# Kernel tuning notes

Measured on AMD Instinct MI355X. Metric: run time of the kernel, lower is better.

## Reference

```python
import jax, jax.numpy as jnp
import numpy as np

V0, V1, C = 64, 128, 128
V = V0 * V1  # product-graph node count = kron eigenvalue count


def setup_inputs() -> dict:
    key = jax.random.key(0)
    ks = jax.random.split(key, 8)
    x = jax.random.normal(ks[0], (V, C), dtype=jnp.float32)
    edge_index = jax.random.randint(ks[1], (2, 100), 0, V)  # unused on spectral path
    L = jnp.zeros((2, 2), dtype=jnp.float32)                # unused on spectral path
    mass = jax.random.uniform(ks[2], (V,), dtype=jnp.float32) + 0.5  # positive lumped mass
    evals0 = jax.random.uniform(ks[3], (V0,), dtype=jnp.float32) * 2.0  # factor-graph eigenvalues >= 0
    evals1 = jax.random.uniform(ks[4], (V1,), dtype=jnp.float32) * 2.0
    evecs = jax.random.normal(ks[5], (V, V), dtype=jnp.float32) / np.float32(np.sqrt(V))
    diffusion_time = jax.random.uniform(ks[6], (2, C), dtype=jnp.float32)  # nn.Parameter [P, C_inout]
    return {
        "x": x, "edge_index": edge_index, "L": L, "mass": mass,
        "evals0": evals0, "evals1": evals1, "evecs": evecs,
        "diffusion_time": diffusion_time,
    }


def reference(x, edge_index, L, mass, evals0, evals1, evecs, diffusion_time):
    # to_basis: project mass-weighted signal onto the spectral basis. [V,C]
    x_spec = evecs.T @ (x * mass[:, None])
    # Per-channel Kronecker diffusion coefficients:
    # kron(exp(-t0[c]*evals0), exp(-t1[c]*evals1)) for each channel c.
    e0 = jnp.exp(-evals0[:, None] * diffusion_time[0][None, :])  # [V0, C]
    e1 = jnp.exp(-evals1[:, None] * diffusion_time[1][None, :])  # [V1, C]
    diffusion_coefs = (e0[:, None, :] * e1[None, :, :]).reshape(V0 * V1, C)  # [V, C]
    # from_basis: back to node domain.
    x_diffuse = evecs @ (diffusion_coefs * x_spec)
    return x_diffuse
```

## Files before the change

### kernel.cpp

```cpp
#include <hip/hip_runtime.h>
#include <stdint.h>

#define V 8192
#define C 128
#define KS 8
#define KCH (V / KS)
#define BK 64
#define NI (KCH / BK)

typedef __attribute__((ext_vector_type(8))) short short8;
typedef __attribute__((ext_vector_type(4))) float floatx4;

static __device__ __forceinline__ unsigned short f2bf(float f) {
    unsigned u = __float_as_uint(f);
    u += 0x7FFF + ((u >> 16) & 1);
    return (unsigned short)(u >> 16);
}

static __device__ __forceinline__ void gload16(const void* g, void* l) {
    __builtin_amdgcn_global_load_lds(
        (const __attribute__((address_space(1))) void*)g,
        (__attribute__((address_space(3))) void*)l, 16, 0, 0);
}
#define SWAIT(s) asm volatile("s_waitcnt " s ::: "memory")
#define SBAR() __builtin_amdgcn_s_barrier()
#define SFENCE() __builtin_amdgcn_sched_barrier(0)

__global__ __launch_bounds__(256) void prep_xmt(const float* __restrict__ x,
                                                const float* __restrict__ mass,
                                                unsigned short* __restrict__ XMT) {
    __shared__ float tile[64][65];
    const int k0 = blockIdx.x * 64;
    const int c0 = blockIdx.y * 64;
    const int t = threadIdx.x;
#pragma unroll
    for (int p = 0; p < 16; ++p) {
        int idx = p * 256 + t;
        int kk = idx >> 6, cc = idx & 63;
        tile[kk][cc] = x[(size_t)(k0 + kk) * C + (c0 + cc)] * mass[k0 + kk];
    }
    __syncthreads();
#pragma unroll
    for (int p = 0; p < 16; ++p) {
        int idx = p * 256 + t;
        int cc = idx >> 6, kk = idx & 63;
        XMT[(size_t)(c0 + cc) * V + (k0 + kk)] = f2bf(tile[kk][cc]);
    }
}

#define MFMA_BODY(pA, pB)                                                           \
    {                                                                               \
        _Pragma("unroll")                                                           \
        for (int kk = 0; kk < BK; kk += 32) {                                       \
            short8 af[4], bfv[4];                                                   \
            _Pragma("unroll")                                                       \
            for (int mi = 0; mi < 4; ++mi) {                                        \
                const int m = wm + mi * 16 + l15;                                   \
                const int cpos = ((kk >> 3) + q) ^ (m & 7);                         \
                af[mi] = *(const short8*)&pA[m * BK + 8 * cpos];                    \
            }                                                                       \
            _Pragma("unroll")                                                       \
            for (int ni = 0; ni < 4; ++ni) {                                        \
                const int n = wn + ni * 16 + l15;                                   \
                const int cpos = ((kk >> 3) + q) ^ (n & 7);                         \
                bfv[ni] = *(const short8*)&pB[n * BK + 8 * cpos];                   \
            }                                                                       \
            _Pragma("unroll")                                                       \
            for (int mi = 0; mi < 4; ++mi)                                          \
                _Pragma("unroll")                                                   \
                for (int ni = 0; ni < 4; ++ni)                                      \
                    acc[mi][ni] = __builtin_amdgcn_mfma_f32_16x16x32_bf16(          \
                        af[mi], bfv[ni], acc[mi][ni], 0, 0, 0);                     \
        }                                                                           \
    }

__global__ __launch_bounds__(256, 2) void gemm1_fused(const unsigned short* __restrict__ XMT,
                                                      const float* __restrict__ E,
                                                      unsigned short* __restrict__ EB,
                                                      float* __restrict__ P1) {
    __shared__ __align__(16) unsigned short ldsA[2][128 * BK];
    __shared__ __align__(16) unsigned short ldsB[2][128 * BK];
    const int bx = blockIdx.x;
    const int ks = bx & (KS - 1);
    const int n0 = (bx >> 3) * 128;
    const int kb = ks * KCH;
    const int t = threadIdx.x;
    const int w = t >> 6, lane = t & 63, q = lane >> 4, l15 = lane & 15;
    const int wm = (w & 1) * 64, wn = (w >> 1) * 64;
    const int lr = lane >> 3;
    const int lch = (lane & 7) ^ lr;
    const int jg = (lane & 7) | (w << 3);
    const int vq = lane >> 3;

    floatx4 acc[4][4] = {};
    float4 er0[8], er1[8];

#define G1_CONV(ER, TI, BUF)                                                        \
    {                                                                               \
        const float* lf = (const float*)ER;                                         \
        unsigned short cv[8][4];                                                    \
        _Pragma("unroll")                                                           \
        for (int rr = 0; rr < 8; ++rr)                                              \
            _Pragma("unroll")                                                       \
            for (int jj = 0; jj < 4; ++jj) cv[rr][jj] = f2bf(lf[rr * 4 + jj]);      \
        _Pragma("unroll")                                                           \
        for (int jj = 0; jj < 4; ++jj) {                                            \
            const int j = jg * 4 + jj;                                              \
            short8 b;                                                               \
            _Pragma("unroll")                                                       \
            for (int rr = 0; rr < 8; ++rr) b[rr] = (short)cv[rr][jj];               \
            *(short8*)&ldsB[BUF][j * BK + (vq ^ (j & 7)) * 8] = b;                  \
        }                                                                           \
        _Pragma("unroll")                                                           \
        for (int rr = 0; rr < 8; ++rr) {                                            \
            ushort4 av;                                                             \
            av.x = cv[rr][0]; av.y = cv[rr][1]; av.z = cv[rr][2]; av.w = cv[rr][3]; \
            *(ushort4*)&EB[(size_t)(kb + (TI) * BK + vq * 8 + rr) * V + n0 + jg * 4] = av; \
        }                                                                           \
    }

#define G1_ELOAD(ER, TI)                                                            \
    {                                                                               \
        const int kk_ = kb + (TI) * BK;                                             \
        _Pragma("unroll")                                                           \
        for (int rr = 0; rr < 8; ++rr)                                              \
            ER[rr] = *(const float4*)&E[(size_t)(kk_ + vq * 8 + rr) * V + n0 + jg * 4]; \
    }

#define G1_GLOADA(TI, BUF)                                                          \
    {                                                                               \
        const int kk_ = kb + (TI) * BK;                                             \
        _Pragma("unroll")                                                           \
        for (int i = 0; i < 4; ++i)                                                 \
            gload16(&XMT[(size_t)(i * 32 + w * 8 + lr) * V + kk_ + 8 * lch],        \
                    &ldsA[BUF][i * 2048 + w * 512]);                                \
    }

    G1_ELOAD(er0, 0);
    G1_GLOADA(0, 0);
    G1_ELOAD(er1, 1);
    G1_CONV(er0, 0, 0);
    SWAIT("vmcnt(16) lgkmcnt(0)");
    SBAR();
    SFENCE();

#define G1_BODY(T, PF_ER, CV_ER)                                                    \
    {                                                                               \
        const int t1 = (T) + 1;                                                     \
        const int t2 = ((T) + 2 < NI) ? (T) + 2 : NI - 1;                           \
        const bool pf = t1 < NI;                                                    \
        if (pf) {                                                                   \
            G1_GLOADA(t1, cur ^ 1);                                                 \
            G1_ELOAD(PF_ER, t2);                                                    \
        }                                                                           \
        SFENCE();                                                                   \
        {                                                                           \
            const unsigned short* pA = ldsA[cur];                                   \
            const unsigned short* pB = ldsB[cur];                                   \
            __builtin_amdgcn_s_setprio(1);                                          \
            MFMA_BODY(pA, pB);                                                      \
            __builtin_amdgcn_s_setprio(0);                                          \
        }                                                                           \
        SFENCE();                                                                   \
        if (pf) {                                                                   \
            G1_CONV(CV_ER, t1, cur ^ 1);                                            \
            SWAIT("vmcnt(16) lgkmcnt(0)");                                          \
            SBAR();                                                                 \
            SFENCE();                                                               \
            cur ^= 1;                                                               \
        }                                                                           \
    }

    int cur = 0;
    for (int tt = 0; tt < NI; tt += 2) {
        G1_BODY(tt, er0, er1);
        G1_BODY(tt + 1, er1, er0);
    }

    float* Pks = P1 + (size_t)ks * C * V;
#pragma unroll
    for (int mi = 0; mi < 4; ++mi) {
        int mrow = wm + mi * 16 + q * 4;
#pragma unroll
        for (int ni = 0; ni < 4; ++ni) {
            int n = n0 + wn + ni * 16 + l15;
#pragma unroll
            for (int r = 0; r < 4; ++r)
                Pks[(size_t)(mrow + r) * V + n] = acc[mi][ni][r];
        }
    }
#undef G1_BODY
#undef G1_CONV
#undef G1_ELOAD
#undef G1_GLOADA
}

__global__ __launch_bounds__(256, 2) void gemm2_fused(const unsigned short* __restrict__ EB,
                                                      const unsigned short* __restrict__ YT,
                                                      float* __restrict__ P2) {
    __shared__ __align__(16) unsigned short ldsA[2][128 * BK];
    __shared__ __align__(16) unsigned short ldsB[2][128 * BK];
    const int bx = blockIdx.x;
    const int ks = bx & (KS - 1);
    const int m0 = (bx >> 3) * 128;
    const int kb = ks * KCH;
    const int t = threadIdx.x;
    const int w = t >> 6, lane = t & 63, q = lane >> 4, l15 = lane & 15;
    const int wm = (w & 1) * 64, wn = (w >> 1) * 64;
    const int lr = lane >> 3;
    const int lch = (lane & 7) ^ lr;

    floatx4 acc[4][4] = {};

#define G2_STAGE(TI, BUF)                                                           \
    {                                                                               \
        const int kk_ = kb + (TI) * BK;                                             \
        _Pragma("unroll")                                                           \
        for (int i = 0; i < 4; ++i)                                                 \
            gload16(&EB[(size_t)(m0 + i * 32 + w * 8 + lr) * V + kk_ + 8 * lch],    \
                    &ldsA[BUF][i * 2048 + w * 512]);                                \
        _Pragma("unroll")                                                           \
        for (int i = 0; i < 4; ++i)                                                 \
            gload16(&YT[(size_t)(i * 32 + w * 8 + lr) * V + kk_ + 8 * lch],         \
                    &ldsB[BUF][i * 2048 + w * 512]);                                \
    }

    G2_STAGE(0, 0);
    SWAIT("vmcnt(0)");
    SBAR();
    SFENCE();

    int cur = 0;
    for (int tt = 0; tt < NI; ++tt) {
        const bool pf = (tt + 1 < NI);
        if (pf) G2_STAGE(tt + 1, cur ^ 1);
        SFENCE();
        {
            const unsigned short* pA = ldsA[cur];
            const unsigned short* pB = ldsB[cur];
            __builtin_amdgcn_s_setprio(1);
            MFMA_BODY(pA, pB);
            __builtin_amdgcn_s_setprio(0);
        }
        SFENCE();
        if (pf) {
            SWAIT("vmcnt(0) lgkmcnt(0)");
            SBAR();
            SFENCE();
            cur ^= 1;
        }
    }
#undef G2_STAGE

    float* Pks = P2 + (size_t)ks * V * C;
#pragma unroll
    for (int mi = 0; mi < 4; ++mi) {
        int mrow = m0 + wm + mi * 16 + q * 4;
#pragma unroll
        for (int ni = 0; ni < 4; ++ni) {
            int n = wn + ni * 16 + l15;
#pragma unroll
            for (int r = 0; r < 4; ++r)
                Pks[(size_t)(mrow + r) * C + n] = acc[mi][ni][r];
        }
    }
}

__global__ __launch_bounds__(256) void red1(const float* __restrict__ P1,
                                            const float* __restrict__ ev0,
                                            const float* __restrict__ ev1,
                                            const float* __restrict__ dt,
                                            unsigned short* __restrict__ YT) {
    int id = blockIdx.x * 256 + threadIdx.x;
    int c = id >> 10;
    int j0 = (id & 1023) * 8;
    float s[8] = {};
#pragma unroll
    for (int ks = 0; ks < KS; ++ks) {
        const float* row = &P1[((size_t)ks * C + c) * V + j0];
        float4 a = *(const float4*)row;
        float4 b = *(const float4*)(row + 4);
        s[0] += a.x; s[1] += a.y; s[2] += a.z; s[3] += a.w;
        s[4] += b.x; s[5] += b.y; s[6] += b.z; s[7] += b.w;
    }
    float t0 = dt[c], t1 = dt[C + c];
    float a0 = ev0[j0 >> 7] * t0;
    short8 yv;
#pragma unroll
    for (int jj = 0; jj < 8; ++jj) {
        float coef = __expf(-(a0 + ev1[(j0 + jj) & 127] * t1));
        yv[jj] = (short)f2bf(s[jj] * coef);
    }
    *(short8*)&YT[(size_t)c * V + j0] = yv;
}

__global__ __launch_bounds__(256) void red2(const float* __restrict__ P2,
                                            float* __restrict__ out) {
    int id = blockIdx.x * 256 + threadIdx.x;
    size_t off = (size_t)id * 4;
    float4 s = {0.f, 0.f, 0.f, 0.f};
#pragma unroll
    for (int ks = 0; ks < KS; ++ks) {
        float4 v = *(const float4*)&P2[(size_t)ks * V * C + off];
        s.x += v.x; s.y += v.y; s.z += v.z; s.w += v.w;
    }
    *(float4*)&out[off] = s;
}

extern "C" void kernel_launch(void* const* d_in, const int* in_sizes, int n_in,
                              void* d_out, int out_size, void* d_ws, size_t ws_size,
                              hipStream_t stream) {
    const float* x    = (const float*)d_in[0];
    const float* mass = (const float*)d_in[3];
    const float* ev0  = (const float*)d_in[4];
    const float* ev1  = (const float*)d_in[5];
    const float* E    = (const float*)d_in[6];
    const float* dt   = (const float*)d_in[7];
    float* out = (float*)d_out;

    unsigned short* XMT = (unsigned short*)d_ws;
    unsigned short* YT  = XMT + (size_t)V * C;
    unsigned short* EB  = YT + (size_t)V * C;
    float* P = (float*)(EB + (size_t)V * V);

    prep_xmt<<<dim3(V / 64, C / 64), 256, 0, stream>>>(x, mass, XMT);
    gemm1_fused<<<(V / 128) * KS, 256, 0, stream>>>(XMT, E, EB, P);
    red1<<<(C * V / 8) / 256, 256, 0, stream>>>(P, ev0, ev1, dt, YT);
    gemm2_fused<<<(V / 128) * KS, 256, 0, stream>>>(EB, YT, P);
    red2<<<(V * C / 4) / 256, 256, 0, stream>>>(P, out);
}
```

Baseline: 451.0 us.

## Replace split-K GEMMs and reductions with full-K narrow-tile GEMMs reading fp32 E

Drops the split-K scheme, the fp32 partial buffers, both reduction kernels and the bf16 copy of evecs. Each GEMM now runs the full K loop over 32-wide output tiles with 512 threads, so 256 blocks cover each GEMM. The diffusion coefficients are applied in the first GEMM's epilogue, and the second GEMM writes the output directly. The trade is that the second GEMM re-reads the fp32 evecs (transposed access) instead of a bf16 copy, and every block runs a longer serial K loop with smaller MFMA tiles per wave.

```diff
diff --git a/kernel.cpp b/kernel.cpp
--- a/kernel.cpp
+++ b/kernel.cpp
@@ -3,10 +3,8 @@
 
 #define V 8192
 #define C 128
-#define KS 8
-#define KCH (V / KS)
 #define BK 64
-#define NI (KCH / BK)
+#define NT (V / BK)
 
 typedef __attribute__((ext_vector_type(8))) short short8;
 typedef __attribute__((ext_vector_type(4))) float floatx4;
@@ -48,123 +46,210 @@
     }
 }
 
-#define MFMA_BODY(pA, pB)                                                           \
-    {                                                                               \
-        _Pragma("unroll")                                                           \
-        for (int kk = 0; kk < BK; kk += 32) {                                       \
-            short8 af[4], bfv[4];                                                   \
-            _Pragma("unroll")                                                       \
-            for (int mi = 0; mi < 4; ++mi) {                                        \
-                const int m = wm + mi * 16 + l15;                                   \
-                const int cpos = ((kk >> 3) + q) ^ (m & 7);                         \
-                af[mi] = *(const short8*)&pA[m * BK + 8 * cpos];                    \
-            }                                                                       \
-            _Pragma("unroll")                                                       \
-            for (int ni = 0; ni < 4; ++ni) {                                        \
-                const int n = wn + ni * 16 + l15;                                   \
-                const int cpos = ((kk >> 3) + q) ^ (n & 7);                         \
-                bfv[ni] = *(const short8*)&pB[n * BK + 8 * cpos];                   \
-            }                                                                       \
-            _Pragma("unroll")                                                       \
-            for (int mi = 0; mi < 4; ++mi)                                          \
-                _Pragma("unroll")                                                   \
-                for (int ni = 0; ni < 4; ++ni)                                      \
-                    acc[mi][ni] = __builtin_amdgcn_mfma_f32_16x16x32_bf16(          \
-                        af[mi], bfv[ni], acc[mi][ni], 0, 0, 0);                     \
-        }                                                                           \
-    }
-
-__global__ __launch_bounds__(256, 2) void gemm1_fused(const unsigned short* __restrict__ XMT,
-                                                      const float* __restrict__ E,
-                                                      unsigned short* __restrict__ EB,
-                                                      float* __restrict__ P1) {
+__global__ __launch_bounds__(512, 2) void gemm1y(const unsigned short* __restrict__ XMT,
+                                                 const float* __restrict__ E,
+                                                 const float* __restrict__ ev0,
+                                                 const float* __restrict__ ev1,
+                                                 const float* __restrict__ dt,
+                                                 unsigned short* __restrict__ YT) {
     __shared__ __align__(16) unsigned short ldsA[2][128 * BK];
-    __shared__ __align__(16) unsigned short ldsB[2][128 * BK];
-    const int bx = blockIdx.x;
-    const int ks = bx & (KS - 1);
-    const int n0 = (bx >> 3) * 128;
-    const int kb = ks * KCH;
+    __shared__ __align__(16) unsigned short ldsB[2][32 * BK];
+    const int j0 = blockIdx.x * 32;
     const int t = threadIdx.x;
     const int w = t >> 6, lane = t & 63, q = lane >> 4, l15 = lane & 15;
-    const int wm = (w & 1) * 64, wn = (w >> 1) * 64;
-    const int lr = lane >> 3;
-    const int lch = (lane & 7) ^ lr;
-    const int jg = (lane & 7) | (w << 3);
-    const int vq = lane >> 3;
-
-    floatx4 acc[4][4] = {};
-    float4 er0[8], er1[8];
-
-#define G1_CONV(ER, TI, BUF)                                                        \
-    {                                                                               \
-        const float* lf = (const float*)ER;                                         \
-        unsigned short cv[8][4];                                                    \
-        _Pragma("unroll")                                                           \
-        for (int rr = 0; rr < 8; ++rr)                                              \
-            _Pragma("unroll")                                                       \
-            for (int jj = 0; jj < 4; ++jj) cv[rr][jj] = f2bf(lf[rr * 4 + jj]);      \
+    const int wr = w >> 1, wc = w & 1;
+    const int lr = lane >> 3, lch = (lane & 7) ^ lr;
+    const int vq4 = t >> 3;
+    const int jgc = t & 7;
+
+    floatx4 acc[2] = {};
+    float4 er0[4], er1[4];
+
+#define G1_GLOADA(TI, BUF)                                                          \
+    {                                                                               \
+        const int kk_ = (TI) * BK;                                                  \
+        _Pragma("unroll")                                                           \
+        for (int i = 0; i < 2; ++i)                                                 \
+            gload16(&XMT[(size_t)(i * 64 + w * 8 + lr) * V + kk_ + 8 * lch],        \
+                    &ldsA[BUF][i * 4096 + w * 512]);                                \
+    }
+#define G1_ELOAD(ER, TI)                                                            \
+    if (w < 2) {                                                                    \
+        const int kk_ = (TI) * BK;                                                  \
+        _Pragma("unroll")                                                           \
+        for (int u = 0; u < 4; ++u)                                                 \
+            ER[u] = *(const float4*)&E[(size_t)(kk_ + vq4 * 4 + u) * V + j0 + jgc * 4]; \
+    }
+#define G1_CONV(ER, BUF)                                                            \
+    if (w < 2) {                                                                    \
         _Pragma("unroll")                                                           \
         for (int jj = 0; jj < 4; ++jj) {                                            \
-            const int j = jg * 4 + jj;                                              \
-            short8 b;                                                               \
-            _Pragma("unroll")                                                       \
-            for (int rr = 0; rr < 8; ++rr) b[rr] = (short)cv[rr][jj];               \
-            *(short8*)&ldsB[BUF][j * BK + (vq ^ (j & 7)) * 8] = b;                  \
-        }                                                                           \
-        _Pragma("unroll")                                                           \
-        for (int rr = 0; rr < 8; ++rr) {                                            \
-            ushort4 av;                                                             \
-            av.x = cv[rr][0]; av.y = cv[rr][1]; av.z = cv[rr][2]; av.w = cv[rr][3]; \
-            *(ushort4*)&EB[(size_t)(kb + (TI) * BK + vq * 8 + rr) * V + n0 + jg * 4] = av; \
-        }                                                                           \
-    }
-
-#define G1_ELOAD(ER, TI)                                                            \
-    {                                                                               \
-        const int kk_ = kb + (TI) * BK;                                             \
-        _Pragma("unroll")                                                           \
-        for (int rr = 0; rr < 8; ++rr)                                              \
-            ER[rr] = *(const float4*)&E[(size_t)(kk_ + vq * 8 + rr) * V + n0 + jg * 4]; \
-    }
-
-#define G1_GLOADA(TI, BUF)                                                          \
-    {                                                                               \
-        const int kk_ = kb + (TI) * BK;                                             \
-        _Pragma("unroll")                                                           \
-        for (int i = 0; i < 4; ++i)                                                 \
-            gload16(&XMT[(size_t)(i * 32 + w * 8 + lr) * V + kk_ + 8 * lch],        \
-                    &ldsA[BUF][i * 2048 + w * 512]);                                \
+            const int j = jgc * 4 + jj;                                             \
+            ushort4 b;                                                              \
+            b.x = f2bf(ER[0][jj]); b.y = f2bf(ER[1][jj]);                           \
+            b.z = f2bf(ER[2][jj]); b.w = f2bf(ER[3][jj]);                           \
+            *(ushort4*)&ldsB[BUF][j * BK + ((vq4 >> 1) ^ (j & 7)) * 8 + (vq4 & 1) * 4] = b; \
+        }                                                                           \
+    }
+#define G1_MFMA(pA, pB)                                                             \
+    {                                                                               \
+        _Pragma("unroll")                                                           \
+        for (int kk = 0; kk < BK; kk += 32) {                                       \
+            short8 af[2], bf1;                                                      \
+            _Pragma("unroll")                                                       \
+            for (int mi = 0; mi < 2; ++mi) {                                        \
+                const int m = wr * 32 + mi * 16 + l15;                              \
+                af[mi] = *(const short8*)&pA[m * BK + 8 * (((kk >> 3) + q) ^ (m & 7))]; \
+            }                                                                       \
+            {                                                                       \
+                const int n = wc * 16 + l15;                                        \
+                bf1 = *(const short8*)&pB[n * BK + 8 * (((kk >> 3) + q) ^ (n & 7))]; \
+            }                                                                       \
+            _Pragma("unroll")                                                       \
+            for (int mi = 0; mi < 2; ++mi)                                          \
+                acc[mi] = __builtin_amdgcn_mfma_f32_16x16x32_bf16(af[mi], bf1, acc[mi], 0, 0, 0); \
+        }                                                                           \
+    }
+#define G1_WAITBAR()                                                                \
+    {                                                                               \
+        if (w < 2) { SWAIT("vmcnt(4) lgkmcnt(0)"); } else { SWAIT("vmcnt(0) lgkmcnt(0)"); } \
+        SBAR();                                                                     \
+        SFENCE();                                                                   \
     }
 
     G1_ELOAD(er0, 0);
     G1_GLOADA(0, 0);
     G1_ELOAD(er1, 1);
-    G1_CONV(er0, 0, 0);
-    SWAIT("vmcnt(16) lgkmcnt(0)");
+    G1_CONV(er0, 0);
+    G1_WAITBAR();
+
+#define G1_BODY(T, PF_ER, CV_ER)                                                    \
+    {                                                                               \
+        const int t1 = (T) + 1;                                                     \
+        const int t2 = ((T) + 2 < NT) ? (T) + 2 : NT - 1;                           \
+        const bool pf = t1 < NT;                                                    \
+        if (pf) {                                                                   \
+            G1_GLOADA(t1, cur ^ 1);                                                 \
+            G1_ELOAD(PF_ER, t2);                                                    \
+        }                                                                           \
+        SFENCE();                                                                   \
+        __builtin_amdgcn_s_setprio(1);                                              \
+        G1_MFMA((&ldsA[cur][0]), (&ldsB[cur][0]));                                  \
+        __builtin_amdgcn_s_setprio(0);                                              \
+        SFENCE();                                                                   \
+        if (pf) {                                                                   \
+            G1_CONV(CV_ER, cur ^ 1);                                                \
+            G1_WAITBAR();                                                           \
+            cur ^= 1;                                                               \
+        }                                                                           \
+    }
+
+    int cur = 0;
+    for (int tt = 0; tt < NT; tt += 2) {
+        G1_BODY(tt, er0, er1);
+        G1_BODY(tt + 1, er1, er0);
+    }
+#undef G1_BODY
+#undef G1_WAITBAR
+#undef G1_MFMA
+#undef G1_CONV
+#undef G1_ELOAD
+#undef G1_GLOADA
+
+    const int jg_ = j0 + wc * 16 + l15;
+    const float a0 = ev0[j0 >> 7];
+    const float e1j = ev1[jg_ & 127];
+#pragma unroll
+    for (int mi = 0; mi < 2; ++mi) {
+#pragma unroll
+        for (int r = 0; r < 4; ++r) {
+            const int c = wr * 32 + mi * 16 + q * 4 + r;
+            const float coef = __expf(-(a0 * dt[c] + e1j * dt[C + c]));
+            YT[(size_t)c * V + jg_] = f2bf(acc[mi][r] * coef);
+        }
+    }
+}
+
+__global__ __launch_bounds__(512, 2) void gemm2o(const float* __restrict__ E,
+                                                 const unsigned short* __restrict__ YT,
+                                                 float* __restrict__ out) {
+    __shared__ __align__(16) unsigned short ldsA[2][32 * BK];
+    __shared__ __align__(16) unsigned short ldsB[2][128 * BK];
+    const int i0 = blockIdx.x * 32;
+    const int t = threadIdx.x;
+    const int w = t >> 6, lane = t & 63, q = lane >> 4, l15 = lane & 15;
+    const int wr = w >> 2, wc = w & 3;
+    const int lr = lane >> 3, lch = (lane & 7) ^ lr;
+    const int arow = t >> 4;
+    const int ach = t & 15;
+
+    floatx4 acc[2] = {};
+    float4 er0, er1;
+
+#define G2_GLOADB(TI, BUF)                                                          \
+    {                                                                               \
+        const int kk_ = (TI) * BK;                                                  \
+        _Pragma("unroll")                                                           \
+        for (int i = 0; i < 2; ++i)                                                 \
+            gload16(&YT[(size_t)(i * 64 + w * 8 + lr) * V + kk_ + 8 * lch],         \
+                    &ldsB[BUF][i * 4096 + w * 512]);                                \
+    }
+#define G2_ELOAD(ER, TI)                                                            \
+    {                                                                               \
+        const int kk_ = (TI) * BK;                                                  \
+        ER = *(const float4*)&E[(size_t)(i0 + arow) * V + kk_ + ach * 4];           \
+    }
+#define G2_CONV(ER, BUF)                                                            \
+    {                                                                               \
+        ushort4 av;                                                                 \
+        av.x = f2bf(ER.x); av.y = f2bf(ER.y); av.z = f2bf(ER.z); av.w = f2bf(ER.w); \
+        *(ushort4*)&ldsA[BUF][arow * BK + ((ach >> 1) ^ (arow & 7)) * 8 + (ach & 1) * 4] = av; \
+    }
+#define G2_MFMA(pA, pB)                                                             \
+    {                                                                               \
+        _Pragma("unroll")                                                           \
+        for (int kk = 0; kk < BK; kk += 32) {                                       \
+            short8 af1, bf[2];                                                      \
+            {                                                                       \
+                const int m = wr * 16 + l15;                                        \
+                af1 = *(const short8*)&pA[m * BK + 8 * (((kk >> 3) + q) ^ (m & 7))]; \
+            }                                                                       \
+            _Pragma("unroll")                                                       \
+            for (int ni = 0; ni < 2; ++ni) {                                        \
+                const int n = wc * 32 + ni * 16 + l15;                              \
+                bf[ni] = *(const short8*)&pB[n * BK + 8 * (((kk >> 3) + q) ^ (n & 7))]; \
+            }                                                                       \
+            _Pragma("unroll")                                                       \
+            for (int ni = 0; ni < 2; ++ni)                                          \
+                acc[ni] = __builtin_amdgcn_mfma_f32_16x16x32_bf16(af1, bf[ni], acc[ni], 0, 0, 0); \
+        }                                                                           \
+    }
+
+    G2_ELOAD(er0, 0);
+    G2_GLOADB(0, 0);
+    G2_ELOAD(er1, 1);
+    G2_CONV(er0, 0);
+    SWAIT("vmcnt(1) lgkmcnt(0)");
     SBAR();
     SFENCE();
 
-#define G1_BODY(T, PF_ER, CV_ER)                                                    \
+#define G2_BODY(T, PF_ER, CV_ER)                                                    \
     {                                                                               \
         const int t1 = (T) + 1;                                                     \
-        const int t2 = ((T) + 2 < NI) ? (T) + 2 : NI - 1;                           \
-        const bool pf = t1 < NI;                                                    \
-        if (pf) {                                                                   \
-            G1_GLOADA(t1, cur ^ 1);                                                 \
-            G1_ELOAD(PF_ER, t2);                                                    \
-        }                                                                           \
-        SFENCE();                                                                   \
-        {                                                                           \
-            const unsigned short* pA = ldsA[cur];                                   \
-            const unsigned short* pB = ldsB[cur];                                   \
-            __builtin_amdgcn_s_setprio(1);                                          \
-            MFMA_BODY(pA, pB);                                                      \
-            __builtin_amdgcn_s_setprio(0);                                          \
-        }                                                                           \
-        SFENCE();                                                                   \
-        if (pf) {                                                                   \
-            G1_CONV(CV_ER, t1, cur ^ 1);                                            \
-            SWAIT("vmcnt(16) lgkmcnt(0)");                                          \
+        const int t2 = ((T) + 2 < NT) ? (T) + 2 : NT - 1;                           \
+        const bool pf = t1 < NT;                                                    \
+        if (pf) {                                                                   \
+            G2_GLOADB(t1, cur ^ 1);                                                 \
+            G2_ELOAD(PF_ER, t2);                                                    \
+        }                                                                           \
+        SFENCE();                                                                   \
+        __builtin_amdgcn_s_setprio(1);                                              \
+        G2_MFMA((&ldsA[cur][0]), (&ldsB[cur][0]));                                  \
+        __builtin_amdgcn_s_setprio(0);                                              \
+        SFENCE();                                                                   \
+        if (pf) {                                                                   \
+            G2_CONV(CV_ER, cur ^ 1);                                                \
+            SWAIT("vmcnt(1) lgkmcnt(0)");                                           \
             SBAR();                                                                 \
             SFENCE();                                                               \
             cur ^= 1;                                                               \
@@ -172,139 +257,23 @@
     }
 
     int cur = 0;
-    for (int tt = 0; tt < NI; tt += 2) {
-        G1_BODY(tt, er0, er1);
-        G1_BODY(tt + 1, er1, er0);
-    }
-
-    float* Pks = P1 + (size_t)ks * C * V;
-#pragma unroll
-    for (int mi = 0; mi < 4; ++mi) {
-        int mrow = wm + mi * 16 + q * 4;
-#pragma unroll
-        for (int ni = 0; ni < 4; ++ni) {
-            int n = n0 + wn + ni * 16 + l15;
-#pragma unroll
-            for (int r = 0; r < 4; ++r)
-                Pks[(size_t)(mrow + r) * V + n] = acc[mi][ni][r];
-        }
-    }
-#undef G1_BODY
-#undef G1_CONV
-#undef G1_ELOAD
-#undef G1_GLOADA
-}
-
-__global__ __launch_bounds__(256, 2) void gemm2_fused(const unsigned short* __restrict__ EB,
-                                                      const unsigned short* __restrict__ YT,
-                                                      float* __restrict__ P2) {
-    __shared__ __align__(16) unsigned short ldsA[2][128 * BK];
-    __shared__ __align__(16) unsigned short ldsB[2][128 * BK];
-    const int bx = blockIdx.x;
-    const int ks = bx & (KS - 1);
-    const int m0 = (bx >> 3) * 128;
-    const int kb = ks * KCH;
-    const int t = threadIdx.x;
-    const int w = t >> 6, lane = t & 63, q = lane >> 4, l15 = lane & 15;
-    const int wm = (w & 1) * 64, wn = (w >> 1) * 64;
-    const int lr = lane >> 3;
-    const int lch = (lane & 7) ^ lr;
-
-    floatx4 acc[4][4] = {};
-
-#define G2_STAGE(TI, BUF)                                                           \
-    {                                                                               \
-        const int kk_ = kb + (TI) * BK;                                             \
-        _Pragma("unroll")                                                           \
-        for (int i = 0; i < 4; ++i)                                                 \
-            gload16(&EB[(size_t)(m0 + i * 32 + w * 8 + lr) * V + kk_ + 8 * lch],    \
-                    &ldsA[BUF][i * 2048 + w * 512]);                                \
-        _Pragma("unroll")                                                           \
-        for (int i = 0; i < 4; ++i)                                                 \
-            gload16(&YT[(size_t)(i * 32 + w * 8 + lr) * V + kk_ + 8 * lch],         \
-                    &ldsB[BUF][i * 2048 + w * 512]);                                \
-    }
-
-    G2_STAGE(0, 0);
-    SWAIT("vmcnt(0)");
-    SBAR();
-    SFENCE();
-
-    int cur = 0;
-    for (int tt = 0; tt < NI; ++tt) {
-        const bool pf = (tt + 1 < NI);
-        if (pf) G2_STAGE(tt + 1, cur ^ 1);
-        SFENCE();
-        {
-            const unsigned short* pA = ldsA[cur];
-            const unsigned short* pB = ldsB[cur];
-            __builtin_amdgcn_s_setprio(1);
-            MFMA_BODY(pA, pB);
-            __builtin_amdgcn_s_setprio(0);
-        }
-        SFENCE();
-        if (pf) {
-            SWAIT("vmcnt(0) lgkmcnt(0)");
-            SBAR();
-            SFENCE();
-            cur ^= 1;
-        }
-    }
-#undef G2_STAGE
-
-    float* Pks = P2 + (size_t)ks * V * C;
-#pragma unroll
-    for (int mi = 0; mi < 4; ++mi) {
-        int mrow = m0 + wm + mi * 16 + q * 4;
-#pragma unroll
-        for (int ni = 0; ni < 4; ++ni) {
-            int n = wn + ni * 16 + l15;
-#pragma unroll
-            for (int r = 0; r < 4; ++r)
-                Pks[(size_t)(mrow + r) * C + n] = acc[mi][ni][r];
-        }
-    }
-}
-
-__global__ __launch_bounds__(256) void red1(const float* __restrict__ P1,
-                                            const float* __restrict__ ev0,
-                                            const float* __restrict__ ev1,
-                                            const float* __restrict__ dt,
-                                            unsigned short* __restrict__ YT) {
-    int id = blockIdx.x * 256 + threadIdx.x;
-    int c = id >> 10;
-    int j0 = (id & 1023) * 8;
-    float s[8] = {};
-#pragma unroll
-    for (int ks = 0; ks < KS; ++ks) {
-        const float* row = &P1[((size_t)ks * C + c) * V + j0];
-        float4 a = *(const float4*)row;
-        float4 b = *(const float4*)(row + 4);
-        s[0] += a.x; s[1] += a.y; s[2] += a.z; s[3] += a.w;
-        s[4] += b.x; s[5] += b.y; s[6] += b.z; s[7] += b.w;
-    }
-    float t0 = dt[c], t1 = dt[C + c];
-    float a0 = ev0[j0 >> 7] * t0;
-    short8 yv;
-#pragma unroll
-    for (int jj = 0; jj < 8; ++jj) {
-        float coef = __expf(-(a0 + ev1[(j0 + jj) & 127] * t1));
-        yv[jj] = (short)f2bf(s[jj] * coef);
-    }
-    *(short8*)&YT[(size_t)c * V + j0] = yv;
-}
-
-__global__ __launch_bounds__(256) void red2(const float* __restrict__ P2,
-                                            float* __restrict__ out) {
-    int id = blockIdx.x * 256 + threadIdx.x;
-    size_t off = (size_t)id * 4;
-    float4 s = {0.f, 0.f, 0.f, 0.f};
-#pragma unroll
-    for (int ks = 0; ks < KS; ++ks) {
-        float4 v = *(const float4*)&P2[(size_t)ks * V * C + off];
-        s.x += v.x; s.y += v.y; s.z += v.z; s.w += v.w;
-    }
-    *(float4*)&out[off] = s;
+    for (int tt = 0; tt < NT; tt += 2) {
+        G2_BODY(tt, er0, er1);
+        G2_BODY(tt + 1, er1, er0);
+    }
+#undef G2_BODY
+#undef G2_MFMA
+#undef G2_CONV
+#undef G2_ELOAD
+#undef G2_GLOADB
+
+#pragma unroll
+    for (int ni = 0; ni < 2; ++ni) {
+#pragma unroll
+        for (int r = 0; r < 4; ++r)
+            out[(size_t)(i0 + wr * 16 + q * 4 + r) * C + wc * 32 + ni * 16 + l15] =
+                acc[ni][r];
+    }
 }
 
 extern "C" void kernel_launch(void* const* d_in, const int* in_sizes, int n_in,
@@ -320,12 +289,8 @@
 
     unsigned short* XMT = (unsigned short*)d_ws;
     unsigned short* YT  = XMT + (size_t)V * C;
-    unsigned short* EB  = YT + (size_t)V * C;
-    float* P = (float*)(EB + (size_t)V * V);
 
     prep_xmt<<<dim3(V / 64, C / 64), 256, 0, stream>>>(x, mass, XMT);
-    gemm1_fused<<<(V / 128) * KS, 256, 0, stream>>>(XMT, E, EB, P);
-    red1<<<(C * V / 8) / 256, 256, 0, stream>>>(P, ev0, ev1, dt, YT);
-    gemm2_fused<<<(V / 128) * KS, 256, 0, stream>>>(EB, YT, P);
-    red2<<<(V * C / 4) / 256, 256, 0, stream>>>(P, out);
-}
+    gemm1y<<<V / 32, 512, 0, stream>>>(XMT, E, ev0, ev1, dt, YT);
+    gemm2o<<<V / 32, 512, 0, stream>>>(E, YT, out);
+}
```

After: 503.6 us. +11.7%, slower.

## Drop bf16 evecs copy; both GEMMs read fp32 evecs directly with KS=4

Applied to the files above, without the earlier changes.

Gemm1 no longer writes a bf16 copy of the 8192x8192 eigenvector matrix. Gemm2 now reads the fp32 matrix itself, converting to bf16 in registers before staging into LDS, the same way gemm1 does. The split-K factor drops from 8 to 4 and the tile width along V shrinks from 128 to 64, so each GEMM still launches 512 blocks and there are fewer partial sums to reduce. This removes a 128 MB bf16 write plus its read-back, but gemm2 now reads 256 MB of fp32 and does the conversion work a second time.

```diff
diff --git a/kernel.cpp b/kernel.cpp
--- a/kernel.cpp
+++ b/kernel.cpp
@@ -3,7 +3,7 @@
 
 #define V 8192
 #define C 128
-#define KS 8
+#define KS 4
 #define KCH (V / KS)
 #define BK 64
 #define NI (KCH / BK)
@@ -48,84 +48,25 @@
     }
 }
 
-#define MFMA_BODY(pA, pB)                                                           \
-    {                                                                               \
-        _Pragma("unroll")                                                           \
-        for (int kk = 0; kk < BK; kk += 32) {                                       \
-            short8 af[4], bfv[4];                                                   \
-            _Pragma("unroll")                                                       \
-            for (int mi = 0; mi < 4; ++mi) {                                        \
-                const int m = wm + mi * 16 + l15;                                   \
-                const int cpos = ((kk >> 3) + q) ^ (m & 7);                         \
-                af[mi] = *(const short8*)&pA[m * BK + 8 * cpos];                    \
-            }                                                                       \
-            _Pragma("unroll")                                                       \
-            for (int ni = 0; ni < 4; ++ni) {                                        \
-                const int n = wn + ni * 16 + l15;                                   \
-                const int cpos = ((kk >> 3) + q) ^ (n & 7);                         \
-                bfv[ni] = *(const short8*)&pB[n * BK + 8 * cpos];                   \
-            }                                                                       \
-            _Pragma("unroll")                                                       \
-            for (int mi = 0; mi < 4; ++mi)                                          \
-                _Pragma("unroll")                                                   \
-                for (int ni = 0; ni < 4; ++ni)                                      \
-                    acc[mi][ni] = __builtin_amdgcn_mfma_f32_16x16x32_bf16(          \
-                        af[mi], bfv[ni], acc[mi][ni], 0, 0, 0);                     \
-        }                                                                           \
-    }
-
-__global__ __launch_bounds__(256, 2) void gemm1_fused(const unsigned short* __restrict__ XMT,
-                                                      const float* __restrict__ E,
-                                                      unsigned short* __restrict__ EB,
-                                                      float* __restrict__ P1) {
+__global__ __launch_bounds__(256, 2) void gemm1_p(const unsigned short* __restrict__ XMT,
+                                                  const float* __restrict__ E,
+                                                  float* __restrict__ P1) {
     __shared__ __align__(16) unsigned short ldsA[2][128 * BK];
-    __shared__ __align__(16) unsigned short ldsB[2][128 * BK];
+    __shared__ __align__(16) unsigned short ldsB[2][64 * BK];
     const int bx = blockIdx.x;
-    const int ks = bx & (KS - 1);
-    const int n0 = (bx >> 3) * 128;
+    const int ks = bx >> 7;
+    const int n0 = (bx & 127) * 64;
     const int kb = ks * KCH;
     const int t = threadIdx.x;
     const int w = t >> 6, lane = t & 63, q = lane >> 4, l15 = lane & 15;
-    const int wm = (w & 1) * 64, wn = (w >> 1) * 64;
+    const int wm = (w & 1) * 64, wn = (w >> 1) * 32;
     const int lr = lane >> 3;
     const int lch = (lane & 7) ^ lr;
-    const int jg = (lane & 7) | (w << 3);
-    const int vq = lane >> 3;
-
-    floatx4 acc[4][4] = {};
-    float4 er0[8], er1[8];
-
-#define G1_CONV(ER, TI, BUF)                                                        \
-    {                                                                               \
-        const float* lf = (const float*)ER;                                         \
-        unsigned short cv[8][4];                                                    \
-        _Pragma("unroll")                                                           \
-        for (int rr = 0; rr < 8; ++rr)                                              \
-            _Pragma("unroll")                                                       \
-            for (int jj = 0; jj < 4; ++jj) cv[rr][jj] = f2bf(lf[rr * 4 + jj]);      \
-        _Pragma("unroll")                                                           \
-        for (int jj = 0; jj < 4; ++jj) {                                            \
-            const int j = jg * 4 + jj;                                              \
-            short8 b;                                                               \
-            _Pragma("unroll")                                                       \
-            for (int rr = 0; rr < 8; ++rr) b[rr] = (short)cv[rr][jj];               \
-            *(short8*)&ldsB[BUF][j * BK + (vq ^ (j & 7)) * 8] = b;                  \
-        }                                                                           \
-        _Pragma("unroll")                                                           \
-        for (int rr = 0; rr < 8; ++rr) {                                            \
-            ushort4 av;                                                             \
-            av.x = cv[rr][0]; av.y = cv[rr][1]; av.z = cv[rr][2]; av.w = cv[rr][3]; \
-            *(ushort4*)&EB[(size_t)(kb + (TI) * BK + vq * 8 + rr) * V + n0 + jg * 4] = av; \
-        }                                                                           \
-    }
-
-#define G1_ELOAD(ER, TI)                                                            \
-    {                                                                               \
-        const int kk_ = kb + (TI) * BK;                                             \
-        _Pragma("unroll")                                                           \
-        for (int rr = 0; rr < 8; ++rr)                                              \
-            ER[rr] = *(const float4*)&E[(size_t)(kk_ + vq * 8 + rr) * V + n0 + jg * 4]; \
-    }
+    const int jc = t & 15;
+    const int vg = t >> 4;
+
+    floatx4 acc[4][2] = {};
+    float4 er0[4], er1[4];
 
 #define G1_GLOADA(TI, BUF)                                                          \
     {                                                                               \
@@ -135,12 +76,53 @@
             gload16(&XMT[(size_t)(i * 32 + w * 8 + lr) * V + kk_ + 8 * lch],        \
                     &ldsA[BUF][i * 2048 + w * 512]);                                \
     }
+#define G1_ELOAD(ER, TI)                                                            \
+    {                                                                               \
+        const int kk_ = kb + (TI) * BK;                                             \
+        _Pragma("unroll")                                                           \
+        for (int u = 0; u < 4; ++u)                                                 \
+            ER[u] = *(const float4*)&E[(size_t)(kk_ + vg * 4 + u) * V + n0 + jc * 4]; \
+    }
+#define G1_CONV(ER, BUF)                                                            \
+    {                                                                               \
+        _Pragma("unroll")                                                           \
+        for (int jj = 0; jj < 4; ++jj) {                                            \
+            const int j = jc * 4 + jj;                                              \
+            ushort4 b;                                                              \
+            b.x = f2bf(ER[0][jj]); b.y = f2bf(ER[1][jj]);                           \
+            b.z = f2bf(ER[2][jj]); b.w = f2bf(ER[3][jj]);                           \
+            *(ushort4*)&ldsB[BUF][j * BK + ((vg >> 1) ^ (j & 7)) * 8 + (vg & 1) * 4] = b; \
+        }                                                                           \
+    }
+#define G1_MFMA(pA, pB)                                                             \
+    {                                                                               \
+        _Pragma("unroll")                                                           \
+        for (int kk = 0; kk < BK; kk += 32) {                                       \
+            short8 af[4], bfv[2];                                                   \
+            _Pragma("unroll")                                                       \
+            for (int mi = 0; mi < 4; ++mi) {                                        \
+                const int m = wm + mi * 16 + l15;                                   \
+                af[mi] = *(const short8*)&pA[m * BK + 8 * (((kk >> 3) + q) ^ (m & 7))]; \
+            }                                                                       \
+            _Pragma("unroll")                                                       \
+            for (int ni = 0; ni < 2; ++ni) {                                        \
+                const int n = wn + ni * 16 + l15;                                   \
+                bfv[ni] = *(const short8*)&pB[n * BK + 8 * (((kk >> 3) + q) ^ (n & 7))]; \
+            }                                                                       \
+            _Pragma("unroll")                                                       \
+            for (int mi = 0; mi < 4; ++mi)                                          \
+                _Pragma("unroll")                                                   \
+                for (int ni = 0; ni < 2; ++ni)                                      \
+                    acc[mi][ni] = __builtin_amdgcn_mfma_f32_16x16x32_bf16(          \
+                        af[mi], bfv[ni], acc[mi][ni], 0, 0, 0);                     \
+        }                                                                           \
+    }
 
     G1_ELOAD(er0, 0);
     G1_GLOADA(0, 0);
     G1_ELOAD(er1, 1);
-    G1_CONV(er0, 0, 0);
-    SWAIT("vmcnt(16) lgkmcnt(0)");
+    G1_CONV(er0, 0);
+    SWAIT("vmcnt(4) lgkmcnt(0)");
     SBAR();
     SFENCE();
 
@@ -154,17 +136,13 @@
             G1_ELOAD(PF_ER, t2);                                                    \
         }                                                                           \
         SFENCE();                                                                   \
-        {                                                                           \
-            const unsigned short* pA = ldsA[cur];                                   \
-            const unsigned short* pB = ldsB[cur];                                   \
-            __builtin_amdgcn_s_setprio(1);                                          \
-            MFMA_BODY(pA, pB);                                                      \
-            __builtin_amdgcn_s_setprio(0);                                          \
-        }                                                                           \
+        __builtin_amdgcn_s_setprio(1);                                              \
+        G1_MFMA((&ldsA[cur][0]), (&ldsB[cur][0]));                                  \
+        __builtin_amdgcn_s_setprio(0);                                              \
         SFENCE();                                                                   \
         if (pf) {                                                                   \
-            G1_CONV(CV_ER, t1, cur ^ 1);                                            \
-            SWAIT("vmcnt(16) lgkmcnt(0)");                                          \
+            G1_CONV(CV_ER, cur ^ 1);                                                \
+            SWAIT("vmcnt(4) lgkmcnt(0)");                                           \
             SBAR();                                                                 \
             SFENCE();                                                               \
             cur ^= 1;                                                               \
@@ -176,85 +154,141 @@
         G1_BODY(tt, er0, er1);
         G1_BODY(tt + 1, er1, er0);
     }
+#undef G1_BODY
+#undef G1_MFMA
+#undef G1_CONV
+#undef G1_ELOAD
+#undef G1_GLOADA
 
     float* Pks = P1 + (size_t)ks * C * V;
 #pragma unroll
     for (int mi = 0; mi < 4; ++mi) {
         int mrow = wm + mi * 16 + q * 4;
 #pragma unroll
-        for (int ni = 0; ni < 4; ++ni) {
+        for (int ni = 0; ni < 2; ++ni) {
             int n = n0 + wn + ni * 16 + l15;
 #pragma unroll
             for (int r = 0; r < 4; ++r)
                 Pks[(size_t)(mrow + r) * V + n] = acc[mi][ni][r];
         }
     }
-#undef G1_BODY
-#undef G1_CONV
-#undef G1_ELOAD
-#undef G1_GLOADA
-}
-
-__global__ __launch_bounds__(256, 2) void gemm2_fused(const unsigned short* __restrict__ EB,
-                                                      const unsigned short* __restrict__ YT,
-                                                      float* __restrict__ P2) {
-    __shared__ __align__(16) unsigned short ldsA[2][128 * BK];
+}
+
+__global__ __launch_bounds__(256, 2) void gemm2_p(const float* __restrict__ E,
+                                                  const unsigned short* __restrict__ YT,
+                                                  float* __restrict__ P2) {
+    __shared__ __align__(16) unsigned short ldsA[2][64 * BK];
     __shared__ __align__(16) unsigned short ldsB[2][128 * BK];
     const int bx = blockIdx.x;
-    const int ks = bx & (KS - 1);
-    const int m0 = (bx >> 3) * 128;
+    const int ks = bx >> 7;
+    const int m0 = (bx & 127) * 64;
     const int kb = ks * KCH;
     const int t = threadIdx.x;
     const int w = t >> 6, lane = t & 63, q = lane >> 4, l15 = lane & 15;
-    const int wm = (w & 1) * 64, wn = (w >> 1) * 64;
+    const int wm = (w & 1) * 32, wn = (w >> 1) * 64;
     const int lr = lane >> 3;
     const int lch = (lane & 7) ^ lr;
-
-    floatx4 acc[4][4] = {};
-
-#define G2_STAGE(TI, BUF)                                                           \
+    const int ach = t & 15;
+    const int arr = t >> 4;
+
+    floatx4 acc[2][4] = {};
+    float4 er0[4], er1[4];
+
+#define G2_GLOADB(TI, BUF)                                                          \
     {                                                                               \
         const int kk_ = kb + (TI) * BK;                                             \
-        _Pragma("unroll")                                                           \
-        for (int i = 0; i < 4; ++i)                                                 \
-            gload16(&EB[(size_t)(m0 + i * 32 + w * 8 + lr) * V + kk_ + 8 * lch],    \
-                    &ldsA[BUF][i * 2048 + w * 512]);                                \
         _Pragma("unroll")                                                           \
         for (int i = 0; i < 4; ++i)                                                 \
             gload16(&YT[(size_t)(i * 32 + w * 8 + lr) * V + kk_ + 8 * lch],         \
                     &ldsB[BUF][i * 2048 + w * 512]);                                \
     }
-
-    G2_STAGE(0, 0);
-    SWAIT("vmcnt(0)");
+#define G2_ELOAD(ER, TI)                                                            \
+    {                                                                               \
+        const int kk_ = kb + (TI) * BK;                                             \
+        _Pragma("unroll")                                                           \
+        for (int u = 0; u < 4; ++u)                                                 \
+            ER[u] = *(const float4*)&E[(size_t)(m0 + arr + 16 * u) * V + kk_ + ach * 4]; \
+    }
+#define G2_CONV(ER, BUF)                                                            \
+    {                                                                               \
+        _Pragma("unroll")                                                           \
+        for (int u = 0; u < 4; ++u) {                                               \
+            const int row = arr + 16 * u;                                           \
+            ushort4 av;                                                             \
+            av.x = f2bf(ER[u].x); av.y = f2bf(ER[u].y);                             \
+            av.z = f2bf(ER[u].z); av.w = f2bf(ER[u].w);                             \
+            *(ushort4*)&ldsA[BUF][row * BK + ((ach >> 1) ^ (row & 7)) * 8 + (ach & 1) * 4] = av; \
+        }                                                                           \
+    }
+#define G2_MFMA(pA, pB)                                                             \
+    {                                                                               \
+        _Pragma("unroll")                                                           \
+        for (int kk = 0; kk < BK; kk += 32) {                                       \
+            short8 af[2], bfv[4];                                                   \
+            _Pragma("unroll")                                                       \
+            for (int mi = 0; mi < 2; ++mi) {                                        \
+                const int m = wm + mi * 16 + l15;                                   \
+                af[mi] = *(const short8*)&pA[m * BK + 8 * (((kk >> 3) + q) ^ (m & 7))]; \
+            }                                                                       \
+            _Pragma("unroll")                                                       \
+            for (int ni = 0; ni < 4; ++ni) {                                        \
+                const int n = wn + ni * 16 + l15;                                   \
+                bfv[ni] = *(const short8*)&pB[n * BK + 8 * (((kk >> 3) + q) ^ (n & 7))]; \
+            }                                                                       \
+            _Pragma("unroll")                                                       \
+            for (int mi = 0; mi < 2; ++mi)                                          \
+                _Pragma("unroll")                                                   \
+                for (int ni = 0; ni < 4; ++ni)                                      \
+                    acc[mi][ni] = __builtin_amdgcn_mfma_f32_16x16x32_bf16(          \
+                        af[mi], bfv[ni], acc[mi][ni], 0, 0, 0);                     \
+        }                                                                           \
+    }
+
+    G2_ELOAD(er0, 0);
+    G2_GLOADB(0, 0);
+    G2_ELOAD(er1, 1);
+    G2_CONV(er0, 0);
+    SWAIT("vmcnt(4) lgkmcnt(0)");
     SBAR();
     SFENCE();
 
+#define G2_BODY(T, PF_ER, CV_ER)                                                    \
+    {                                                                               \
+        const int t1 = (T) + 1;                                                     \
+        const int t2 = ((T) + 2 < NI) ? (T) + 2 : NI - 1;                           \
+        const bool pf = t1 < NI;                                                    \
+        if (pf) {                                                                   \
+            G2_GLOADB(t1, cur ^ 1);                                                 \
+            G2_ELOAD(PF_ER, t2);                                                    \
+        }                                                                           \
+        SFENCE();                                                                   \
+        __builtin_amdgcn_s_setprio(1);                                              \
+        G2_MFMA((&ldsA[cur][0]), (&ldsB[cur][0]));                                  \
+        __builtin_amdgcn_s_setprio(0);                                              \
+        SFENCE();                                                                   \
+        if (pf) {                                                                   \
+            G2_CONV(CV_ER, cur ^ 1);                                                \
+            SWAIT("vmcnt(4) lgkmcnt(0)");                                           \
+            SBAR();                                                                 \
+            SFENCE();                                                               \
+            cur ^= 1;                                                               \
+        }                                                                           \
+    }
+
     int cur = 0;
-    for (int tt = 0; tt < NI; ++tt) {
-        const bool pf = (tt + 1 < NI);
-        if (pf) G2_STAGE(tt + 1, cur ^ 1);
-        SFENCE();
-        {
-            const unsigned short* pA = ldsA[cur];
-            const unsigned short* pB = ldsB[cur];
-            __builtin_amdgcn_s_setprio(1);
-            MFMA_BODY(pA, pB);
-            __builtin_amdgcn_s_setprio(0);
-        }
-        SFENCE();
-        if (pf) {
-            SWAIT("vmcnt(0) lgkmcnt(0)");
-            SBAR();
-            SFENCE();
-            cur ^= 1;
-        }
-    }
-#undef G2_STAGE
+    for (int tt = 0; tt < NI; tt += 2) {
+        G2_BODY(tt, er0, er1);
+        G2_BODY(tt + 1, er1, er0);
+    }
+#undef G2_BODY
+#undef G2_MFMA
+#undef G2_CONV
+#undef G2_ELOAD
+#undef G2_GLOADB
 
     float* Pks = P2 + (size_t)ks * V * C;
 #pragma unroll
-    for (int mi = 0; mi < 4; ++mi) {
+    for (int mi = 0; mi < 2; ++mi) {
         int mrow = m0 + wm + mi * 16 + q * 4;
 #pragma unroll
         for (int ni = 0; ni < 4; ++ni) {
@@ -320,12 +354,11 @@
 
     unsigned short* XMT = (unsigned short*)d_ws;
     unsigned short* YT  = XMT + (size_t)V * C;
-    unsigned short* EB  = YT + (size_t)V * C;
-    float* P = (float*)(EB + (size_t)V * V);
+    float* P = (float*)(YT + (size_t)V * C);
 
     prep_xmt<<<dim3(V / 64, C / 64), 256, 0, stream>>>(x, mass, XMT);
-    gemm1_fused<<<(V / 128) * KS, 256, 0, stream>>>(XMT, E, EB, P);
+    gemm1_p<<<(V / 64) * KS, 256, 0, stream>>>(XMT, E, P);
     red1<<<(C * V / 8) / 256, 256, 0, stream>>>(P, ev0, ev1, dt, YT);
-    gemm2_fused<<<(V / 128) * KS, 256, 0, stream>>>(EB, YT, P);
+    gemm2_p<<<(V / 64) * KS, 256, 0, stream>>>(E, YT, P);
     red2<<<(V * C / 4) / 256, 256, 0, stream>>>(P, out);
 }
```

Result: no change. 443.3 us (-1.7%).
